# Kernel tuning notes

Hardware: AMD Instinct MI355X
Metric: run time of the kernel (lower is better)

## Reference

```python
import jax, jax.numpy as jnp
import numpy as np

BL = 512              # block length (init kwarg bl)
HALF = BL // 2
WIN = BL + 2 * HALF   # window width seen by each query block
Q_DIM = K_DIM = V_DIM = 256
R1 = R2 = R3 = 2
CQ, CK, CV = Q_DIM // R1, K_DIM // R2, V_DIM // R3


def setup_inputs() -> dict:
    key = jax.random.key(0)
    ks = jax.random.split(key, 9)
    B, L = 1, 131072
    def w(k, shape, fan):
        return (jax.random.normal(k, shape, jnp.float32) / np.float32(np.sqrt(fan)))
    return {
        "x1": jax.random.normal(ks[0], (B, Q_DIM, L), jnp.float32),
        "mask": jnp.ones((B, 1, L), jnp.float32),
        "Wq": w(ks[1], (CQ, Q_DIM), Q_DIM), "bq": jnp.zeros((CQ,), jnp.float32),
        "Wk": w(ks[2], (CK, K_DIM), K_DIM), "bk": jnp.zeros((CK,), jnp.float32),
        "Wv": w(ks[3], (CV, V_DIM), V_DIM), "bv": jnp.zeros((CV,), jnp.float32),
        "Wo": w(ks[4], (V_DIM, CV), CV),   "bo": jnp.zeros((V_DIM,), jnp.float32),
    }


def conv1x1(W, b, x):
    # nn.Conv1d(kernel_size=1): (B, Cin, L) -> (B, Cout, L)
    return jnp.einsum('oc,bcl->bol', W, x) + b[None, :, None]


def _sliding_window_att(q, k, v, mask):
    B, cq, L = q.shape
    cv = v.shape[1]
    nb = L // BL  # L chosen divisible by BL (remainder-pad branch is a no-op)
    # per-frame padding mask, (B,1,L)
    pm = jnp.broadcast_to(mask[:, 0:1, :], (B, 1, L))
    # blocked queries: (B*nb, cq, BL)
    qb = q.reshape(B, cq, nb, BL).transpose(0, 2, 1, 3).reshape(B * nb, cq, BL)
    # pad k / v / mask by HALF zeros on both sides, then take overlapping windows
    kp = jnp.pad(k, ((0, 0), (0, 0), (HALF, HALF)))
    vp = jnp.pad(v, ((0, 0), (0, 0), (HALF, HALF)))
    mp = jnp.pad(pm, ((0, 0), (0, 0), (HALF, HALF)))
    idx = np.arange(nb)[:, None] * BL + np.arange(WIN)[None, :]
    kb = kp[:, :, idx].transpose(0, 2, 1, 3).reshape(B * nb, -1, WIN)
    vb = vp[:, :, idx].transpose(0, 2, 1, 3).reshape(B * nb, -1, WIN)
    mb = mp[:, :, idx].transpose(0, 2, 1, 3).reshape(B * nb, 1, WIN)
    # construct_window_mask: loop sets window_mask[:, :, i:i+BL] = 1 for i in [0,BL),
    # whose union is columns [0, 2*BL-1) for ALL rows (faithful to the given code).
    wm = (jnp.arange(WIN) < (2 * BL - 1)).astype(q.dtype)[None, None, :]
    fm = wm * mb  # final mask, broadcasts over the BL query rows
    # scalar_dot_att with log-mask trick
    energy = jnp.einsum('ncl,ncw->nlw', qb, kb) / np.float32(np.sqrt(cq))
    att = jax.nn.softmax(energy + jnp.log(fm + 1e-6), axis=-1) * fm
    out = jnp.einsum('ncw,nlw->ncl', vb, att)  # (B*nb, cv, BL)
    return out, nb, cv


def reference(x1, mask, Wq, bq, Wk, bk, Wv, bv, Wo, bo):
    B, _, L = x1.shape
    q = conv1x1(Wq, bq, x1)
    k = conv1x1(Wk, bk, x1)
    v = conv1x1(Wv, bv, x1)
    out, nb, cv = _sliding_window_att(q, k, v, mask)
    out = conv1x1(Wo, bo, jax.nn.relu(out))  # (B*nb, V_DIM, BL)
    out = out.reshape(B, nb, V_DIM, BL).transpose(0, 2, 1, 3).reshape(B, V_DIM, nb * BL)
    out = out[:, :, :L]
    return out * mask[:, 0:1, :]
```

## Files before the change

### kernel.cpp

```cpp
#include <hip/hip_runtime.h>
#include <math.h>

#define LTOT 131072

typedef unsigned short u16;
typedef unsigned int   u32;
typedef __attribute__((ext_vector_type(8))) short bf16x8;
typedef __attribute__((ext_vector_type(4))) short bf16x4;
typedef __attribute__((ext_vector_type(4))) float f32x4;

__device__ __forceinline__ u16 f2b(float f) {
  union { float f; u32 u; } v; v.f = f;
  u32 r = v.u + 0x7fffu + ((v.u >> 16) & 1u);
  return (u16)(r >> 16);
}

__device__ __forceinline__ u32 cvt_pk(float lo, float hi) {
  u32 r;
  asm("v_cvt_pk_bf16_f32 %0, %1, %2" : "=v"(r) : "v"(lo), "v"(hi));
  return r;
}

__device__ __forceinline__ bf16x8 pack_bp(const f32x4 a, const f32x4 b) {
  union { u32 w[4]; bf16x8 v; } u;
  u.w[0] = cvt_pk(a[0], a[1]);
  u.w[1] = cvt_pk(a[2], a[3]);
  u.w[2] = cvt_pk(b[0], b[1]);
  u.w[3] = cvt_pk(b[2], b[3]);
  return u.v;
}

__device__ __forceinline__ int sxt_addr(int row, int g) {
  return (row << 8) + (((g) ^ (row & 7)) << 3);
}

__global__ __launch_bounds__(512) void k_qkv(
    const float* __restrict__ x1,
    const float* __restrict__ Wq, const float* __restrict__ bq,
    const float* __restrict__ Wk, const float* __restrict__ bk,
    const float* __restrict__ Wv, const float* __restrict__ bv,
    const float* __restrict__ Wo,
    u16* __restrict__ scratch, u16* __restrict__ WoB)
{
  __shared__ __align__(16) u16 sXT[128 * 256];

  const int tid  = threadIdx.x;
  const int lane = tid & 63;
  const int wv   = tid >> 6;
  const int lr   = lane & 15;
  const int lg   = lane >> 4;
  const int l0   = blockIdx.x << 7;

  {
    const int cl = (tid & 63) << 1;
    const int kq = tid >> 6;
#pragma unroll
    for (int k8 = 0; k8 < 4; ++k8) {
      const int k0 = kq * 32 + k8 * 8;
      float2 v[8];
#pragma unroll
      for (int j = 0; j < 8; ++j)
        v[j] = *reinterpret_cast<const float2*>(x1 + (size_t)(k0 + j) * LTOT + l0 + cl);
      union { u16 h[8]; bf16x8 b; } p0, p1;
#pragma unroll
      for (int j = 0; j < 8; ++j) {
        p0.h[j] = f2b(v[j].x);
        p1.h[j] = f2b(v[j].y);
      }
      const int g = k0 >> 3;
      *reinterpret_cast<bf16x8*>(&sXT[sxt_addr(cl,     g)]) = p0.b;
      *reinterpret_cast<bf16x8*>(&sXT[sxt_addr(cl + 1, g)]) = p1.b;
    }
  }

  if (blockIdx.x == 0) {
    for (int idx = tid; idx < 32768; idx += 512) WoB[idx] = f2b(Wo[idx]);
  }
  __syncthreads();

  const float rs = 0.1275174468f;

#pragma unroll
  for (int wb = 0; wb < 2; ++wb) {
    const float* Wsel = wb ? Wk : Wq;
    const float* bsel = wb ? bk : bq;
    const int c = (wv << 4) + lr;

    bf16x8 bw[8];
    {
      const float* wrow = Wsel + (size_t)c * 256 + (lg << 3);
#pragma unroll
      for (int kc = 0; kc < 8; ++kc) {
        float4 wa = *reinterpret_cast<const float4*>(wrow + kc * 32);
        float4 wc = *reinterpret_cast<const float4*>(wrow + kc * 32 + 4);
        union { u16 h[8]; bf16x8 b; } u;
        u.h[0] = f2b(wa.x); u.h[1] = f2b(wa.y); u.h[2] = f2b(wa.z); u.h[3] = f2b(wa.w);
        u.h[4] = f2b(wc.x); u.h[5] = f2b(wc.y); u.h[6] = f2b(wc.z); u.h[7] = f2b(wc.w);
        bw[kc] = u.b;
      }
    }

    f32x4 acc[8];
#pragma unroll
    for (int mt = 0; mt < 8; ++mt) acc[mt] = (f32x4){0.f, 0.f, 0.f, 0.f};
#pragma unroll
    for (int kc = 0; kc < 8; ++kc) {
      const int g = (kc << 2) + lg;
#pragma unroll
      for (int mt = 0; mt < 8; ++mt) {
        bf16x8 a = *reinterpret_cast<const bf16x8*>(&sXT[sxt_addr((mt << 4) + lr, g)]);
        acc[mt] = __builtin_amdgcn_mfma_f32_16x16x32_bf16(bw[kc], a, acc[mt], 0, 0, 0);
      }
    }

    const int c0 = (wv << 4) + (lg << 2);
    float4 b4 = *reinterpret_cast<const float4*>(bsel + c0);
    const float bb[4] = {b4.x, b4.y, b4.z, b4.w};
    const float scale = wb ? 1.f : rs;
    u16* dst = scratch + (size_t)wb * 128 * LTOT;
#pragma unroll
    for (int mt = 0; mt < 8; ++mt) {
      const int l = l0 + (mt << 4) + lr;
      union { u16 h[4]; uint2 v; } s;
#pragma unroll
      for (int r = 0; r < 4; ++r)
        s.h[r] = f2b((acc[mt][r] + bb[r]) * scale);
      *reinterpret_cast<uint2*>(dst + (size_t)l * 128 + c0) = s.v;
    }
  }

  {
    const int c = (wv << 4) + lr;
    bf16x8 aw[8];
    {
      const float* wrow = Wv + (size_t)c * 256 + (lg << 3);
#pragma unroll
      for (int kc = 0; kc < 8; ++kc) {
        float4 wa = *reinterpret_cast<const float4*>(wrow + kc * 32);
        float4 wc = *reinterpret_cast<const float4*>(wrow + kc * 32 + 4);
        union { u16 h[8]; bf16x8 b; } u;
        u.h[0] = f2b(wa.x); u.h[1] = f2b(wa.y); u.h[2] = f2b(wa.z); u.h[3] = f2b(wa.w);
        u.h[4] = f2b(wc.x); u.h[5] = f2b(wc.y); u.h[6] = f2b(wc.z); u.h[7] = f2b(wc.w);
        aw[kc] = u.b;
      }
    }

    f32x4 acc[8];
#pragma unroll
    for (int nt = 0; nt < 8; ++nt) acc[nt] = (f32x4){0.f, 0.f, 0.f, 0.f};
#pragma unroll
    for (int kc = 0; kc < 8; ++kc) {
      const int g = (kc << 2) + lg;
#pragma unroll
      for (int nt = 0; nt < 8; ++nt) {
        bf16x8 b = *reinterpret_cast<const bf16x8*>(&sXT[sxt_addr((nt << 4) + lr, g)]);
        acc[nt] = __builtin_amdgcn_mfma_f32_16x16x32_bf16(b, aw[kc], acc[nt], 0, 0, 0);
      }
    }

    const float bias = bv[c];
    u16* dstv = scratch + (size_t)256 * LTOT + (size_t)c * LTOT;
#pragma unroll
    for (int nt = 0; nt < 8; ++nt) {
      const int p0 = l0 + (nt << 4) + (lg << 2);
      union { u16 h[4]; uint2 v; } s;
#pragma unroll
      for (int r = 0; r < 4; ++r)
        s.h[r] = f2b(acc[nt][r] + bias);
      *reinterpret_cast<uint2*>(dstv + p0) = s.v;
    }
  }
}

__global__ __launch_bounds__(256, 2) void k_attn(
    const u16* __restrict__ scratch,
    const float* __restrict__ mask,
    u16* __restrict__ attT)
{
  __shared__ __align__(16) unsigned char smem[44032];
  u16*   sKT = (u16*)smem;
  u16*   sV  = (u16*)(smem + 17408);
  float* sLF = (float*)(smem + 35840);
  float* sFM = (float*)(smem + 39936);

  const int tid  = threadIdx.x;
  const int lane = tid & 63;
  const int wv   = tid >> 6;
  const int lr   = lane & 15;
  const int lg   = lane >> 4;
  const int lid  = ((int)blockIdx.x & 7) * 128 + ((int)blockIdx.x >> 3);
  const int lq0  = lid << 7;
  const int p_base = (lq0 >> 9) * 512 - 256;
  const int wq0  = lq0 + wv * 32;

  const u16* QT = scratch;
  const u16* KT = scratch + (size_t)128 * LTOT;
  const u16* Vp = scratch + (size_t)256 * LTOT;

  for (int idx = tid; idx < 1024; idx += 256) {
    int p = p_base + idx;
    float fmv = 0.f;
    if (idx < 1023 && (unsigned)p < (unsigned)LTOT) fmv = mask[p];
    sFM[idx] = fmv;
    sLF[idx] = log2f(fmv + 1e-6f);
  }

  bf16x8 aQ0[4], aQ1[4];
#pragma unroll
  for (int kc = 0; kc < 4; ++kc) {
    aQ0[kc] = *reinterpret_cast<const bf16x8*>(
        QT + (size_t)(wq0 + lr) * 128 + kc * 32 + (lg << 3));
    aQ1[kc] = *reinterpret_cast<const bf16x8*>(
        QT + (size_t)(wq0 + 16 + lr) * 128 + kc * 32 + (lg << 3));
  }

  float m0 = -INFINITY, m1 = -INFINITY;
  f32x4 d40 = (f32x4){0.f, 0.f, 0.f, 0.f};
  f32x4 d41 = (f32x4){0.f, 0.f, 0.f, 0.f};
  f32x4 accO0[8], accO1[8];
#pragma unroll
  for (int cm = 0; cm < 8; ++cm) {
    accO0[cm] = (f32x4){0.f, 0.f, 0.f, 0.f};
    accO1[cm] = (f32x4){0.f, 0.f, 0.f, 0.f};
  }

  uint4 rk[4], rv[4];
  {
    const int p0 = p_base;
#pragma unroll
    for (int j = 0; j < 4; ++j) {
      int idx = tid + j * 256;
      int row = idx >> 4, ch = (idx & 15) << 3;
      int p = p0 + row;
      rk[j] = make_uint4(0u, 0u, 0u, 0u);
      if ((unsigned)p < (unsigned)LTOT)
        rk[j] = *reinterpret_cast<const uint4*>(KT + (size_t)p * 128 + ch);
      int c = idx >> 3, w = (idx & 7) << 3;
      int pp = p0 + w;
      rv[j] = make_uint4(0u, 0u, 0u, 0u);
      if ((unsigned)pp < (unsigned)LTOT)
        rv[j] = *reinterpret_cast<const uint4*>(Vp + (size_t)c * LTOT + pp);
    }
  }
#pragma unroll
  for (int j = 0; j < 4; ++j) {
    int idx = tid + j * 256;
    int row = idx >> 4, ch = (idx & 15) << 3;
    *reinterpret_cast<uint4*>(&sKT[row * 136 + ch]) = rk[j];
    int c = idx >> 3, w = (idx & 7) << 3;
    *reinterpret_cast<uint4*>(&sV[c * 72 + w]) = rv[j];
  }
  __syncthreads();

  for (int it = 0; it < 16; ++it) {
    if (it < 15) {
      const int p0 = p_base + (it + 1) * 64;
#pragma unroll
      for (int j = 0; j < 4; ++j) {
        int idx = tid + j * 256;
        int row = idx >> 4, ch = (idx & 15) << 3;
        int p = p0 + row;
        rk[j] = make_uint4(0u, 0u, 0u, 0u);
        if ((unsigned)p < (unsigned)LTOT)
          rk[j] = *reinterpret_cast<const uint4*>(KT + (size_t)p * 128 + ch);
        int c = idx >> 3, w = (idx & 7) << 3;
        int pp = p0 + w;
        rv[j] = make_uint4(0u, 0u, 0u, 0u);
        if ((unsigned)pp < (unsigned)LTOT)
          rv[j] = *reinterpret_cast<const uint4*>(Vp + (size_t)c * LTOT + pp);
      }
    }

    f32x4 e0[4], e1[4];
#pragma unroll
    for (int nt = 0; nt < 4; ++nt) {
      e0[nt] = (f32x4){0.f, 0.f, 0.f, 0.f};
      e1[nt] = (f32x4){0.f, 0.f, 0.f, 0.f};
    }
#pragma unroll
    for (int kc = 0; kc < 4; ++kc) {
      const int ko = kc * 32 + (lg << 3);
#pragma unroll
      for (int nt = 0; nt < 4; ++nt) {
        bf16x8 bk = *reinterpret_cast<const bf16x8*>(&sKT[(nt * 16 + lr) * 136 + ko]);
        e0[nt] = __builtin_amdgcn_mfma_f32_16x16x32_bf16(bk, aQ0[kc], e0[nt], 0, 0, 0);
        e1[nt] = __builtin_amdgcn_mfma_f32_16x16x32_bf16(bk, aQ1[kc], e1[nt], 0, 0, 0);
      }
    }

    const int wbase = it * 64 + (lg << 2);
    f32x4 lf[4], fmv[4];
#pragma unroll
    for (int nt = 0; nt < 4; ++nt) {
      lf[nt]  = *reinterpret_cast<const f32x4*>(&sLF[wbase + nt * 16]);
      fmv[nt] = *reinterpret_cast<const f32x4*>(&sFM[wbase + nt * 16]);
      e0[nt] += lf[nt];
      e1[nt] += lf[nt];
    }

    bf16x8 bpA0, bpA1;
    {
      float lmax = e0[0][0];
#pragma unroll
      for (int nt = 0; nt < 4; ++nt)
#pragma unroll
        for (int r = 0; r < 4; ++r) if (nt || r) lmax = fmaxf(lmax, e0[nt][r]);
      if (__any(lmax > m0 + 12.0f)) {
        float rmax = lmax;
        rmax = fmaxf(rmax, __shfl_xor(rmax, 16));
        rmax = fmaxf(rmax, __shfl_xor(rmax, 32));
        float mnew = fmaxf(m0, rmax);
        float fs = exp2f(m0 - mnew);
        d40 *= fs;
#pragma unroll
        for (int cm = 0; cm < 8; ++cm) accO0[cm] *= fs;
        m0 = mnew;
      }
      f32x4 pn[4];
#pragma unroll
      for (int nt = 0; nt < 4; ++nt) {
        f32x4 pd;
#pragma unroll
        for (int r = 0; r < 4; ++r) pd[r] = exp2f(e0[nt][r] - m0);
        d40 += pd;
        pn[nt] = pd * fmv[nt];
      }
      bpA0 = pack_bp(pn[0], pn[1]);
      bpA1 = pack_bp(pn[2], pn[3]);
    }

    bf16x8 bpB0, bpB1;
    {
      float lmax = e1[0][0];
#pragma unroll
      for (int nt = 0; nt < 4; ++nt)
#pragma unroll
        for (int r = 0; r < 4; ++r) if (nt || r) lmax = fmaxf(lmax, e1[nt][r]);
      if (__any(lmax > m1 + 12.0f)) {
        float rmax = lmax;
        rmax = fmaxf(rmax, __shfl_xor(rmax, 16));
        rmax = fmaxf(rmax, __shfl_xor(rmax, 32));
        float mnew = fmaxf(m1, rmax);
        float fs = exp2f(m1 - mnew);
        d41 *= fs;
#pragma unroll
        for (int cm = 0; cm < 8; ++cm) accO1[cm] *= fs;
        m1 = mnew;
      }
      f32x4 pn[4];
#pragma unroll
      for (int nt = 0; nt < 4; ++nt) {
        f32x4 pd;
#pragma unroll
        for (int r = 0; r < 4; ++r) pd[r] = exp2f(e1[nt][r] - m1);
        d41 += pd;
        pn[nt] = pd * fmv[nt];
      }
      bpB0 = pack_bp(pn[0], pn[1]);
      bpB1 = pack_bp(pn[2], pn[3]);
    }

#pragma unroll
    for (int k2 = 0; k2 < 2; ++k2) {
      const bf16x8 pA = k2 ? bpA1 : bpA0;
      const bf16x8 pB = k2 ? bpB1 : bpB0;
      const int vo = k2 * 32 + (lg << 2);
#pragma unroll
      for (int cm = 0; cm < 8; ++cm) {
        const u16* vr = &sV[(cm * 16 + lr) * 72 + vo];
        bf16x4 v0 = *reinterpret_cast<const bf16x4*>(vr);
        bf16x4 v1 = *reinterpret_cast<const bf16x4*>(vr + 16);
        bf16x8 av = __builtin_shufflevector(v0, v1, 0, 1, 2, 3, 4, 5, 6, 7);
        accO0[cm] = __builtin_amdgcn_mfma_f32_16x16x32_bf16(av, pA, accO0[cm], 0, 0, 0);
        accO1[cm] = __builtin_amdgcn_mfma_f32_16x16x32_bf16(av, pB, accO1[cm], 0, 0, 0);
      }
    }

    __syncthreads();
    if (it < 15) {
#pragma unroll
      for (int j = 0; j < 4; ++j) {
        int idx = tid + j * 256;
        int row = idx >> 4, ch = (idx & 15) << 3;
        *reinterpret_cast<uint4*>(&sKT[row * 136 + ch]) = rk[j];
        int c = idx >> 3, w = (idx & 7) << 3;
        *reinterpret_cast<uint4*>(&sV[c * 72 + w]) = rv[j];
      }
    }
    __syncthreads();
  }

  float ds0 = d40[0] + d40[1] + d40[2] + d40[3];
  ds0 += __shfl_xor(ds0, 16);
  ds0 += __shfl_xor(ds0, 32);
  const float rd0 = 1.f / ds0;
  float ds1 = d41[0] + d41[1] + d41[2] + d41[3];
  ds1 += __shfl_xor(ds1, 16);
  ds1 += __shfl_xor(ds1, 32);
  const float rd1 = 1.f / ds1;

  u16* sT = (u16*)smem + wv * 2176;
#pragma unroll
  for (int cm = 0; cm < 8; ++cm) {
    float o0 = fmaxf(accO0[cm][0] * rd0, 0.f);
    float o1 = fmaxf(accO0[cm][1] * rd0, 0.f);
    float o2 = fmaxf(accO0[cm][2] * rd0, 0.f);
    float o3 = fmaxf(accO0[cm][3] * rd0, 0.f);
    uint2 pk = make_uint2(cvt_pk(o0, o1), cvt_pk(o2, o3));
    *reinterpret_cast<uint2*>(&sT[lr * 136 + cm * 16 + (lg << 2)]) = pk;
  }
  for (int idx = lane; idx < 256; idx += 64) {
    int row = idx >> 4, ch = (idx & 15) << 3;
    uint4 v = *reinterpret_cast<const uint4*>(&sT[row * 136 + ch]);
    *reinterpret_cast<uint4*>(attT + (size_t)(wq0 + row) * 128 + ch) = v;
  }
#pragma unroll
  for (int cm = 0; cm < 8; ++cm) {
    float o0 = fmaxf(accO1[cm][0] * rd1, 0.f);
    float o1 = fmaxf(accO1[cm][1] * rd1, 0.f);
    float o2 = fmaxf(accO1[cm][2] * rd1, 0.f);
    float o3 = fmaxf(accO1[cm][3] * rd1, 0.f);
    uint2 pk = make_uint2(cvt_pk(o0, o1), cvt_pk(o2, o3));
    *reinterpret_cast<uint2*>(&sT[lr * 136 + cm * 16 + (lg << 2)]) = pk;
  }
  for (int idx = lane; idx < 256; idx += 64) {
    int row = idx >> 4, ch = (idx & 15) << 3;
    uint4 v = *reinterpret_cast<const uint4*>(&sT[row * 136 + ch]);
    *reinterpret_cast<uint4*>(attT + (size_t)(wq0 + 16 + row) * 128 + ch) = v;
  }
}

__device__ __forceinline__ int sa_addr(int row, int g) {
  return (row << 7) + (((g) ^ (row & 7)) << 3);
}

__global__ __launch_bounds__(512) void k_out(
    const u16* __restrict__ attT, const u16* __restrict__ WoB,
    const float* __restrict__ bo, const float* __restrict__ mask,
    float* __restrict__ out)
{
  __shared__ __align__(16) u16 sA[128 * 128];

  const int tid  = threadIdx.x;
  const int lane = tid & 63;
  const int wv   = tid >> 6;
  const int lr   = lane & 15;
  const int lg   = lane >> 4;
  const int l0   = blockIdx.x << 7;

  for (int idx = tid; idx < 2048; idx += 512) {
    int row = idx >> 4, g = idx & 15;
    uint4 v = *reinterpret_cast<const uint4*>(attT + (size_t)(l0 + row) * 128 + (g << 3));
    *reinterpret_cast<uint4*>(&sA[sa_addr(row, g)]) = v;
  }
  __syncthreads();

  const int ob = wv << 5;
  f32x4 acc[2][8];
#pragma unroll
  for (int mt = 0; mt < 2; ++mt)
#pragma unroll
    for (int nt = 0; nt < 8; ++nt) acc[mt][nt] = (f32x4){0.f, 0.f, 0.f, 0.f};

#pragma unroll
  for (int kc = 0; kc < 4; ++kc) {
    bf16x8 a[2], b[8];
#pragma unroll
    for (int mt = 0; mt < 2; ++mt)
      a[mt] = *reinterpret_cast<const bf16x8*>(
          WoB + (size_t)(ob + mt * 16 + lr) * 128 + kc * 32 + (lg << 3));
    const int g = (kc << 2) + lg;
#pragma unroll
    for (int nt = 0; nt < 8; ++nt)
      b[nt] = *reinterpret_cast<const bf16x8*>(&sA[sa_addr(nt * 16 + lr, g)]);
#pragma unroll
    for (int mt = 0; mt < 2; ++mt)
#pragma unroll
      for (int nt = 0; nt < 8; ++nt)
        acc[mt][nt] = __builtin_amdgcn_mfma_f32_16x16x32_bf16(a[mt], b[nt], acc[mt][nt], 0, 0, 0);
  }

#pragma unroll
  for (int mt = 0; mt < 2; ++mt) {
    const int o0 = ob + mt * 16 + (lg << 2);
    float4 b4 = *reinterpret_cast<const float4*>(bo + o0);
#pragma unroll
    for (int nt = 0; nt < 8; ++nt) {
      const int l = l0 + nt * 16 + lr;
      const float mk = mask[l];
      out[(size_t)(o0 + 0) * LTOT + l] = (acc[mt][nt][0] + b4.x) * mk;
      out[(size_t)(o0 + 1) * LTOT + l] = (acc[mt][nt][1] + b4.y) * mk;
      out[(size_t)(o0 + 2) * LTOT + l] = (acc[mt][nt][2] + b4.z) * mk;
      out[(size_t)(o0 + 3) * LTOT + l] = (acc[mt][nt][3] + b4.w) * mk;
    }
  }
}

extern "C" void kernel_launch(void* const* d_in, const int* in_sizes, int n_in,
                              void* d_out, int out_size, void* d_ws, size_t ws_size,
                              hipStream_t stream) {
  (void)in_sizes; (void)n_in; (void)out_size; (void)ws_size;
  const float* x1   = (const float*)d_in[0];
  const float* mask = (const float*)d_in[1];
  const float* Wq   = (const float*)d_in[2];
  const float* bq   = (const float*)d_in[3];
  const float* Wk   = (const float*)d_in[4];
  const float* bk   = (const float*)d_in[5];
  const float* Wv   = (const float*)d_in[6];
  const float* bv   = (const float*)d_in[7];
  const float* Wo   = (const float*)d_in[8];
  const float* bo   = (const float*)d_in[9];

  u16* scratch = (u16*)d_out;
  u16* attT    = (u16*)d_ws;
  u16* WoB     = attT + (size_t)128 * LTOT;
  float* out   = (float*)d_out;

  hipLaunchKernelGGL(k_qkv, dim3(1024), dim3(512), 0, stream,
                     x1, Wq, bq, Wk, bk, Wv, bv, Wo, scratch, WoB);
  hipLaunchKernelGGL(k_attn, dim3(1024), dim3(256), 0, stream,
                     scratch, mask, attT);
  hipLaunchKernelGGL(k_out, dim3(1024), dim3(512), 0, stream,
                     attT, WoB, bo, mask, out);
}
```

Baseline: 228.4 us.

## Fuse output projection into attention epilogue when workspace is large enough

Adds a templated fused path in which each attention wave applies ReLU, packs its output into bf16 MFMA operands, and multiplies by a pre-permuted bf16 copy of Wo read from global memory. It then adds the bias, applies the mask and writes the final fp32 output directly. This removes the attT intermediate round trip and the separate k_out launch. Because the final output is now written while other blocks still read K/V, QKV scratch moves from the output buffer into the workspace, so the fused path only runs when ws_size can hold it; otherwise the old three-kernel path is kept. The cost is a heavier attention epilogue: repeated Wo loads per wave, more register pressure under launch_bounds(256,2), and strided fp32 stores.

```diff
diff --git a/kernel.cpp b/kernel.cpp
--- a/kernel.cpp
+++ b/kernel.cpp
@@ -40,7 +40,7 @@
     const float* __restrict__ Wk, const float* __restrict__ bk,
     const float* __restrict__ Wv, const float* __restrict__ bv,
     const float* __restrict__ Wo,
-    u16* __restrict__ scratch, u16* __restrict__ WoB)
+    u16* __restrict__ scratch, u16* __restrict__ WoB, u16* __restrict__ WoF)
 {
   __shared__ __align__(16) u16 sXT[128 * 256];
 
@@ -74,7 +74,13 @@
   }
 
   if (blockIdx.x == 0) {
-    for (int idx = tid; idx < 32768; idx += 512) WoB[idx] = f2b(Wo[idx]);
+    for (int idx = tid; idx < 32768; idx += 512) {
+      WoB[idx] = f2b(Wo[idx]);
+      int o = idx >> 7, s = idx & 127;
+      int ks = s >> 5, g = (s >> 3) & 3, j = s & 7;
+      int c = ks * 32 + g * 4 + (j & 3) + 16 * (j >> 2);
+      WoF[idx] = f2b(Wo[o * 128 + c]);
+    }
   }
   __syncthreads();
 
@@ -172,10 +178,14 @@
   }
 }
 
+template<int FUSED>
 __global__ __launch_bounds__(256, 2) void k_attn(
     const u16* __restrict__ scratch,
     const float* __restrict__ mask,
-    u16* __restrict__ attT)
+    u16* __restrict__ attT,
+    float* __restrict__ out,
+    const u16* __restrict__ WoF,
+    const float* __restrict__ bo)
 {
   __shared__ __align__(16) unsigned char smem[44032];
   u16*   sKT = (u16*)smem;
@@ -399,34 +409,74 @@
   ds1 += __shfl_xor(ds1, 32);
   const float rd1 = 1.f / ds1;
 
-  u16* sT = (u16*)smem + wv * 2176;
-#pragma unroll
-  for (int cm = 0; cm < 8; ++cm) {
-    float o0 = fmaxf(accO0[cm][0] * rd0, 0.f);
-    float o1 = fmaxf(accO0[cm][1] * rd0, 0.f);
-    float o2 = fmaxf(accO0[cm][2] * rd0, 0.f);
-    float o3 = fmaxf(accO0[cm][3] * rd0, 0.f);
-    uint2 pk = make_uint2(cvt_pk(o0, o1), cvt_pk(o2, o3));
-    *reinterpret_cast<uint2*>(&sT[lr * 136 + cm * 16 + (lg << 2)]) = pk;
-  }
-  for (int idx = lane; idx < 256; idx += 64) {
-    int row = idx >> 4, ch = (idx & 15) << 3;
-    uint4 v = *reinterpret_cast<const uint4*>(&sT[row * 136 + ch]);
-    *reinterpret_cast<uint4*>(attT + (size_t)(wq0 + row) * 128 + ch) = v;
-  }
-#pragma unroll
-  for (int cm = 0; cm < 8; ++cm) {
-    float o0 = fmaxf(accO1[cm][0] * rd1, 0.f);
-    float o1 = fmaxf(accO1[cm][1] * rd1, 0.f);
-    float o2 = fmaxf(accO1[cm][2] * rd1, 0.f);
-    float o3 = fmaxf(accO1[cm][3] * rd1, 0.f);
-    uint2 pk = make_uint2(cvt_pk(o0, o1), cvt_pk(o2, o3));
-    *reinterpret_cast<uint2*>(&sT[lr * 136 + cm * 16 + (lg << 2)]) = pk;
-  }
-  for (int idx = lane; idx < 256; idx += 64) {
-    int row = idx >> 4, ch = (idx & 15) << 3;
-    uint4 v = *reinterpret_cast<const uint4*>(&sT[row * 136 + ch]);
-    *reinterpret_cast<uint4*>(attT + (size_t)(wq0 + 16 + row) * 128 + ch) = v;
+  if (FUSED) {
+#pragma unroll
+    for (int grp = 0; grp < 2; ++grp) {
+      const f32x4* aO = grp ? accO1 : accO0;
+      const float  rd = grp ? rd1 : rd0;
+      const size_t l  = (size_t)(wq0 + grp * 16 + lr);
+      const float  mk = mask[l];
+      u16 ob[8][4];
+#pragma unroll
+      for (int cm = 0; cm < 8; ++cm)
+#pragma unroll
+        for (int r = 0; r < 4; ++r)
+          ob[cm][r] = f2b(fmaxf(aO[cm][r] * rd, 0.f));
+      bf16x8 pb[4];
+#pragma unroll
+      for (int ks = 0; ks < 4; ++ks) {
+        union { u16 h[8]; bf16x8 b; } u;
+#pragma unroll
+        for (int j = 0; j < 4; ++j) { u.h[j] = ob[2 * ks][j]; u.h[4 + j] = ob[2 * ks + 1][j]; }
+        pb[ks] = u.b;
+      }
+#pragma unroll
+      for (int ot = 0; ot < 16; ++ot) {
+        f32x4 acc = (f32x4){0.f, 0.f, 0.f, 0.f};
+#pragma unroll
+        for (int ks = 0; ks < 4; ++ks) {
+          bf16x8 aW = *reinterpret_cast<const bf16x8*>(
+              WoF + (size_t)(ot * 16 + lr) * 128 + ks * 32 + (lg << 3));
+          acc = __builtin_amdgcn_mfma_f32_16x16x32_bf16(aW, pb[ks], acc, 0, 0, 0);
+        }
+        const int o0 = ot * 16 + (lg << 2);
+        float4 b4 = *reinterpret_cast<const float4*>(bo + o0);
+        out[(size_t)(o0 + 0) * LTOT + l] = (acc[0] + b4.x) * mk;
+        out[(size_t)(o0 + 1) * LTOT + l] = (acc[1] + b4.y) * mk;
+        out[(size_t)(o0 + 2) * LTOT + l] = (acc[2] + b4.z) * mk;
+        out[(size_t)(o0 + 3) * LTOT + l] = (acc[3] + b4.w) * mk;
+      }
+    }
+  } else {
+    u16* sT = (u16*)smem + wv * 2176;
+#pragma unroll
+    for (int cm = 0; cm < 8; ++cm) {
+      float o0 = fmaxf(accO0[cm][0] * rd0, 0.f);
+      float o1 = fmaxf(accO0[cm][1] * rd0, 0.f);
+      float o2 = fmaxf(accO0[cm][2] * rd0, 0.f);
+      float o3 = fmaxf(accO0[cm][3] * rd0, 0.f);
+      uint2 pk = make_uint2(cvt_pk(o0, o1), cvt_pk(o2, o3));
+      *reinterpret_cast<uint2*>(&sT[lr * 136 + cm * 16 + (lg << 2)]) = pk;
+    }
+    for (int idx = lane; idx < 256; idx += 64) {
+      int row = idx >> 4, ch = (idx & 15) << 3;
+      uint4 v = *reinterpret_cast<const uint4*>(&sT[row * 136 + ch]);
+      *reinterpret_cast<uint4*>(attT + (size_t)(wq0 + row) * 128 + ch) = v;
+    }
+#pragma unroll
+    for (int cm = 0; cm < 8; ++cm) {
+      float o0 = fmaxf(accO1[cm][0] * rd1, 0.f);
+      float o1 = fmaxf(accO1[cm][1] * rd1, 0.f);
+      float o2 = fmaxf(accO1[cm][2] * rd1, 0.f);
+      float o3 = fmaxf(accO1[cm][3] * rd1, 0.f);
+      uint2 pk = make_uint2(cvt_pk(o0, o1), cvt_pk(o2, o3));
+      *reinterpret_cast<uint2*>(&sT[lr * 136 + cm * 16 + (lg << 2)]) = pk;
+    }
+    for (int idx = lane; idx < 256; idx += 64) {
+      int row = idx >> 4, ch = (idx & 15) << 3;
+      uint4 v = *reinterpret_cast<const uint4*>(&sT[row * 136 + ch]);
+      *reinterpret_cast<uint4*>(attT + (size_t)(wq0 + 16 + row) * 128 + ch) = v;
+    }
   }
 }
 
@@ -499,7 +549,7 @@
 extern "C" void kernel_launch(void* const* d_in, const int* in_sizes, int n_in,
                               void* d_out, int out_size, void* d_ws, size_t ws_size,
                               hipStream_t stream) {
-  (void)in_sizes; (void)n_in; (void)out_size; (void)ws_size;
+  (void)in_sizes; (void)n_in; (void)out_size;
   const float* x1   = (const float*)d_in[0];
   const float* mask = (const float*)d_in[1];
   const float* Wq   = (const float*)d_in[2];
@@ -510,16 +560,29 @@
   const float* bv   = (const float*)d_in[7];
   const float* Wo   = (const float*)d_in[8];
   const float* bo   = (const float*)d_in[9];
-
-  u16* scratch = (u16*)d_out;
-  u16* attT    = (u16*)d_ws;
-  u16* WoB     = attT + (size_t)128 * LTOT;
-  float* out   = (float*)d_out;
-
-  hipLaunchKernelGGL(k_qkv, dim3(1024), dim3(512), 0, stream,
-                     x1, Wq, bq, Wk, bk, Wv, bv, Wo, scratch, WoB);
-  hipLaunchKernelGGL(k_attn, dim3(1024), dim3(256), 0, stream,
-                     scratch, mask, attT);
-  hipLaunchKernelGGL(k_out, dim3(1024), dim3(512), 0, stream,
-                     attT, WoB, bo, mask, out);
-}
+  float* out = (float*)d_out;
+
+  const size_t needF = ((size_t)384 * LTOT + 2 * 32768) * sizeof(u16);
+  const bool fused = ws_size >= needF;
+
+  if (fused) {
+    u16* scratch = (u16*)d_ws;
+    u16* WoF = scratch + (size_t)384 * LTOT;
+    u16* WoB = WoF + 32768;
+    hipLaunchKernelGGL(k_qkv, dim3(1024), dim3(512), 0, stream,
+                       x1, Wq, bq, Wk, bk, Wv, bv, Wo, scratch, WoB, WoF);
+    hipLaunchKernelGGL(k_attn<1>, dim3(1024), dim3(256), 0, stream,
+                       scratch, mask, (u16*)nullptr, out, WoF, bo);
+  } else {
+    u16* scratch = (u16*)d_out;
+    u16* attT = (u16*)d_ws;
+    u16* WoB  = attT + (size_t)128 * LTOT;
+    u16* WoF  = WoB + 32768;
+    hipLaunchKernelGGL(k_qkv, dim3(1024), dim3(512), 0, stream,
+                       x1, Wq, bq, Wk, bk, Wv, bv, Wo, scratch, WoB, WoF);
+    hipLaunchKernelGGL(k_attn<0>, dim3(1024), dim3(256), 0, stream,
+                       scratch, mask, attT, out, WoF, bo);
+    hipLaunchKernelGGL(k_out, dim3(1024), dim3(512), 0, stream,
+                       attT, WoB, bo, mask, out);
+  }
+}
```

New measurement: 267.7 us. 1.17x slower.

## Precompute bf16 weights in a prep kernel and raise attention occupancy

Applied to the files above, without the earlier changes.

Adds a small prep kernel that converts Wq/Wk/Wv/Wo to bf16 once, so each k_qkv block loads bf16 weight fragments directly instead of converting fp32 weights per block. In k_attn, the mask and log-mask tables are stored in shared memory as bf16 to shrink LDS, and launch bounds are raised to 4 blocks per CU. This trades an extra kernel launch and bf16 rounding of the log-mask (about -19.9, where exactness matters little) for less redundant conversion work and higher attention occupancy, at the risk of register spills under the tighter register budget.

```diff
diff --git a/kernel.cpp b/kernel.cpp
--- a/kernel.cpp
+++ b/kernel.cpp
@@ -13,6 +13,10 @@
   union { float f; u32 u; } v; v.f = f;
   u32 r = v.u + 0x7fffu + ((v.u >> 16) & 1u);
   return (u16)(r >> 16);
+}
+
+__device__ __forceinline__ float b2f(u16 h) {
+  union { u32 u; float f; } v; v.u = ((u32)h) << 16; return v.f;
 }
 
 __device__ __forceinline__ u32 cvt_pk(float lo, float hi) {
@@ -30,17 +34,29 @@
   return u.v;
 }
 
+__global__ __launch_bounds__(256) void k_prep(
+    const float* __restrict__ Wq, const float* __restrict__ Wk,
+    const float* __restrict__ Wv, const float* __restrict__ Wo,
+    u16* __restrict__ WB)
+{
+  for (int idx = blockIdx.x * 256 + threadIdx.x; idx < 131072;
+       idx += gridDim.x * 256) {
+    int sel = idx >> 15, off = idx & 32767;
+    const float* s = (sel == 0) ? Wq : (sel == 1) ? Wk : (sel == 2) ? Wv : Wo;
+    WB[idx] = f2b(s[off]);
+  }
+}
+
 __device__ __forceinline__ int sxt_addr(int row, int g) {
   return (row << 8) + (((g) ^ (row & 7)) << 3);
 }
 
 __global__ __launch_bounds__(512) void k_qkv(
     const float* __restrict__ x1,
-    const float* __restrict__ Wq, const float* __restrict__ bq,
-    const float* __restrict__ Wk, const float* __restrict__ bk,
-    const float* __restrict__ Wv, const float* __restrict__ bv,
-    const float* __restrict__ Wo,
-    u16* __restrict__ scratch, u16* __restrict__ WoB)
+    const u16* __restrict__ WB,
+    const float* __restrict__ bq, const float* __restrict__ bk,
+    const float* __restrict__ bv,
+    u16* __restrict__ scratch)
 {
   __shared__ __align__(16) u16 sXT[128 * 256];
 
@@ -72,33 +88,21 @@
       *reinterpret_cast<bf16x8*>(&sXT[sxt_addr(cl + 1, g)]) = p1.b;
     }
   }
-
-  if (blockIdx.x == 0) {
-    for (int idx = tid; idx < 32768; idx += 512) WoB[idx] = f2b(Wo[idx]);
-  }
   __syncthreads();
 
   const float rs = 0.1275174468f;
 
 #pragma unroll
   for (int wb = 0; wb < 2; ++wb) {
-    const float* Wsel = wb ? Wk : Wq;
+    const u16* Wsel = WB + wb * 32768;
     const float* bsel = wb ? bk : bq;
     const int c = (wv << 4) + lr;
 
     bf16x8 bw[8];
-    {
-      const float* wrow = Wsel + (size_t)c * 256 + (lg << 3);
-#pragma unroll
-      for (int kc = 0; kc < 8; ++kc) {
-        float4 wa = *reinterpret_cast<const float4*>(wrow + kc * 32);
-        float4 wc = *reinterpret_cast<const float4*>(wrow + kc * 32 + 4);
-        union { u16 h[8]; bf16x8 b; } u;
-        u.h[0] = f2b(wa.x); u.h[1] = f2b(wa.y); u.h[2] = f2b(wa.z); u.h[3] = f2b(wa.w);
-        u.h[4] = f2b(wc.x); u.h[5] = f2b(wc.y); u.h[6] = f2b(wc.z); u.h[7] = f2b(wc.w);
-        bw[kc] = u.b;
-      }
-    }
+#pragma unroll
+    for (int kc = 0; kc < 8; ++kc)
+      bw[kc] = *reinterpret_cast<const bf16x8*>(
+          Wsel + (size_t)c * 256 + kc * 32 + (lg << 3));
 
     f32x4 acc[8];
 #pragma unroll
@@ -130,20 +134,13 @@
   }
 
   {
+    const u16* Wsel = WB + 65536;
     const int c = (wv << 4) + lr;
     bf16x8 aw[8];
-    {
-      const float* wrow = Wv + (size_t)c * 256 + (lg << 3);
-#pragma unroll
-      for (int kc = 0; kc < 8; ++kc) {
-        float4 wa = *reinterpret_cast<const float4*>(wrow + kc * 32);
-        float4 wc = *reinterpret_cast<const float4*>(wrow + kc * 32 + 4);
-        union { u16 h[8]; bf16x8 b; } u;
-        u.h[0] = f2b(wa.x); u.h[1] = f2b(wa.y); u.h[2] = f2b(wa.z); u.h[3] = f2b(wa.w);
-        u.h[4] = f2b(wc.x); u.h[5] = f2b(wc.y); u.h[6] = f2b(wc.z); u.h[7] = f2b(wc.w);
-        aw[kc] = u.b;
-      }
-    }
+#pragma unroll
+    for (int kc = 0; kc < 8; ++kc)
+      aw[kc] = *reinterpret_cast<const bf16x8*>(
+          Wsel + (size_t)c * 256 + kc * 32 + (lg << 3));
 
     f32x4 acc[8];
 #pragma unroll
@@ -172,16 +169,16 @@
   }
 }
 
-__global__ __launch_bounds__(256, 2) void k_attn(
+__global__ __launch_bounds__(256, 4) void k_attn(
     const u16* __restrict__ scratch,
     const float* __restrict__ mask,
     u16* __restrict__ attT)
 {
-  __shared__ __align__(16) unsigned char smem[44032];
-  u16*   sKT = (u16*)smem;
-  u16*   sV  = (u16*)(smem + 17408);
-  float* sLF = (float*)(smem + 35840);
-  float* sFM = (float*)(smem + 39936);
+  __shared__ __align__(16) unsigned char smem[39936];
+  u16*   sKT  = (u16*)smem;
+  u16*   sV   = (u16*)(smem + 17408);
+  u16*   sLFh = (u16*)(smem + 35840);
+  u16*   sFMh = (u16*)(smem + 37888);
 
   const int tid  = threadIdx.x;
   const int lane = tid & 63;
@@ -201,8 +198,8 @@
     int p = p_base + idx;
     float fmv = 0.f;
     if (idx < 1023 && (unsigned)p < (unsigned)LTOT) fmv = mask[p];
-    sFM[idx] = fmv;
-    sLF[idx] = log2f(fmv + 1e-6f);
+    sFMh[idx] = f2b(fmv);
+    sLFh[idx] = f2b(log2f(fmv + 1e-6f));
   }
 
   bf16x8 aQ0[4], aQ1[4];
@@ -292,8 +289,14 @@
     f32x4 lf[4], fmv[4];
 #pragma unroll
     for (int nt = 0; nt < 4; ++nt) {
-      lf[nt]  = *reinterpret_cast<const f32x4*>(&sLF[wbase + nt * 16]);
-      fmv[nt] = *reinterpret_cast<const f32x4*>(&sFM[wbase + nt * 16]);
+      union { u16 h[4]; uint2 v; } L, F;
+      L.v = *reinterpret_cast<const uint2*>(&sLFh[wbase + nt * 16]);
+      F.v = *reinterpret_cast<const uint2*>(&sFMh[wbase + nt * 16]);
+#pragma unroll
+      for (int r = 0; r < 4; ++r) {
+        lf[nt][r]  = b2f(L.h[r]);
+        fmv[nt][r] = b2f(F.h[r]);
+      }
       e0[nt] += lf[nt];
       e1[nt] += lf[nt];
     }
@@ -513,11 +516,14 @@
 
   u16* scratch = (u16*)d_out;
   u16* attT    = (u16*)d_ws;
-  u16* WoB     = attT + (size_t)128 * LTOT;
+  u16* WB      = attT + (size_t)128 * LTOT;
+  u16* WoB     = WB + 98304;
   float* out   = (float*)d_out;
 
+  hipLaunchKernelGGL(k_prep, dim3(128), dim3(256), 0, stream,
+                     Wq, Wk, Wv, Wo, WB);
   hipLaunchKernelGGL(k_qkv, dim3(1024), dim3(512), 0, stream,
-                     x1, Wq, bq, Wk, bk, Wv, bv, Wo, scratch, WoB);
+                     x1, WB, bq, bk, bv, scratch);
   hipLaunchKernelGGL(k_attn, dim3(1024), dim3(256), 0, stream,
                      scratch, mask, attT);
   hipLaunchKernelGGL(k_out, dim3(1024), dim3(512), 0, stream,
```

After: 717.0 us. +213.9%, slower.
